# Optimization experiments

Measured on AMD Instinct MI355X. Metric: run time of the kernel, lower is better.

## Reference

```python
import jax, jax.numpy as jnp
import numpy as np

B, T = 64, 1024
S, O = 512, 32000


def setup_inputs() -> dict:
    key = jax.random.key(0)
    k1, k2, k3, k4 = jax.random.split(key, 4)
    return {
        "observations": jax.random.randint(k1, (B, T), 0, O),
        "state_transitions": jax.random.normal(k2, (S, S), dtype=jnp.float32),
        "observation_transitions": jax.random.normal(k3, (S, O), dtype=jnp.float32),
        "prior_states": jax.random.normal(k4, (S,), dtype=jnp.float32),
    }


def reference(observations, state_transitions, observation_transitions, prior_states):
    # Precompute log-softmaxed parameters once (torch code recomputed per step).
    log_trans = jax.nn.log_softmax(state_transitions, axis=-1)        # [S, S]
    log_obs = jax.nn.log_softmax(observation_transitions, axis=-1)    # [S, O]
    log_prior = jax.nn.log_softmax(prior_states)                      # [S]

    b = observations.shape[0]
    # torch code appends a terminal observation 0 at the end of each sequence
    obs_seq = jnp.concatenate(
        [observations, jnp.zeros((b, 1), dtype=observations.dtype)], axis=1
    )  # [B, T+1]

    # alpha_0[b, s] = log_obs[s, o_0(b)] + log_prior[s]
    alpha0 = log_obs[:, obs_seq[:, 0]].T + log_prior  # [B, S]

    def step(alpha, obs_t):
        # alpha[b, i] -> pred[b, j] = logsumexp_i(alpha[b, i] + log_trans[i, j])
        pred = jax.nn.logsumexp(alpha[:, :, None] + log_trans[None, :, :], axis=1)  # [B, S]
        new_alpha = log_obs[:, obs_t].T + pred  # [B, S]
        return new_alpha, None

    alpha, _ = jax.lax.scan(step, alpha0, obs_seq[:, 1:].T)  # scan over T steps
    return jax.nn.logsumexp(alpha, axis=1)  # [B]
```

## Files before the change

kernel.cpp:

```cpp
#include <hip/hip_runtime.h>
#include <hip/hip_bf16.h>
#include <cstdint>

#define SS 512
#define OBS_N 32000
#define TT 1024
#define BB 64

#define RPW 24
#define LDS_I2 64
#define LPW 8

typedef _Float16 h2 __attribute__((ext_vector_type(2)));

static __device__ __forceinline__ float wave_max(float v) {
#pragma unroll
  for (int m = 32; m >= 1; m >>= 1) v = fmaxf(v, __shfl_xor(v, m, 64));
  return v;
}
static __device__ __forceinline__ float wave_sum(float v) {
#pragma unroll
  for (int m = 32; m >= 1; m >>= 1) v += __shfl_xor(v, m, 64);
  return v;
}

__global__ __launch_bounds__(256) void prep_obs_lse(const float* __restrict__ ot,
                                                    float* __restrict__ lse) {
  const int s = blockIdx.x;
  const int tid = threadIdx.x;
  const float4* row = (const float4*)(ot + (size_t)s * OBS_N);
  __shared__ float redm[4];
  __shared__ float reds[4];

  float m = -INFINITY;
  for (int k = tid; k < OBS_N / 4; k += 256) {
    float4 v = row[k];
    m = fmaxf(m, fmaxf(fmaxf(v.x, v.y), fmaxf(v.z, v.w)));
  }
  m = wave_max(m);
  if ((tid & 63) == 0) redm[tid >> 6] = m;
  __syncthreads();
  m = fmaxf(fmaxf(redm[0], redm[1]), fmaxf(redm[2], redm[3]));

  float ssum = 0.f;
  for (int k = tid; k < OBS_N / 4; k += 256) {
    float4 v = row[k];
    ssum += __expf(v.x - m) + __expf(v.y - m) + __expf(v.z - m) + __expf(v.w - m);
  }
  ssum = wave_sum(ssum);
  if ((tid & 63) == 0) reds[tid >> 6] = ssum;
  __syncthreads();
  if (tid == 0) {
    float s4 = reds[0] + reds[1] + reds[2] + reds[3];
    lse[s] = m + __logf(s4);
  }
}

__global__ __launch_bounds__(512) void prep_trans(const float* __restrict__ st,
                                                  uint32_t* __restrict__ EP) {
  const int r = blockIdx.x;
  const int j = threadIdx.x;
  const int wv = j >> 6;
  float a0 = st[(size_t)(2 * r) * SS + j];
  float a1 = st[(size_t)(2 * r + 1) * SS + j];

  __shared__ float w0[8], w1[8], s0a[8], s1a[8];
  float m0 = wave_max(a0), m1 = wave_max(a1);
  if ((j & 63) == 0) { w0[wv] = m0; w1[wv] = m1; }
  __syncthreads();
  m0 = w0[0]; m1 = w1[0];
#pragma unroll
  for (int q = 1; q < 8; ++q) { m0 = fmaxf(m0, w0[q]); m1 = fmaxf(m1, w1[q]); }

  float e0 = __expf(a0 - m0), e1 = __expf(a1 - m1);
  float s0 = wave_sum(e0), s1 = wave_sum(e1);
  if ((j & 63) == 0) { s0a[wv] = s0; s1a[wv] = s1; }
  __syncthreads();
  s0 = 0.f; s1 = 0.f;
#pragma unroll
  for (int q = 0; q < 8; ++q) { s0 += s0a[q]; s1 += s1a[q]; }

  _Float16 h0 = (_Float16)(e0 / s0);
  _Float16 h1 = (_Float16)(e1 / s1);
  uint32_t u = ((uint32_t)__builtin_bit_cast(unsigned short, h1) << 16) |
               (uint32_t)__builtin_bit_cast(unsigned short, h0);
  EP[(size_t)r * SS + j] = u;
}

__global__ __launch_bounds__(512) void prep_prior(const float* __restrict__ pr,
                                                  float* __restrict__ lp) {
  const int j = threadIdx.x;
  const int wv = j >> 6;
  float a = pr[j];
  __shared__ float wm[8], ws[8];
  float m = wave_max(a);
  if ((j & 63) == 0) wm[wv] = m;
  __syncthreads();
  m = wm[0];
#pragma unroll
  for (int q = 1; q < 8; ++q) m = fmaxf(m, wm[q]);
  float e = __expf(a - m);
  float s = wave_sum(e);
  if ((j & 63) == 0) ws[wv] = s;
  __syncthreads();
  s = 0.f;
#pragma unroll
  for (int q = 0; q < 8; ++q) s += ws[q];
  lp[j] = a - m - __logf(s);
}

__global__ __launch_bounds__(512, 2) void hmm_main(
    const uint32_t* __restrict__ EP, const float* __restrict__ lse_obs,
    const float* __restrict__ lp, const int* __restrict__ obs,
    const float* __restrict__ ot, float* __restrict__ out) {
  __shared__ uint32_t eL[LDS_I2][64][8];
  __shared__ uint32_t ph32[SS / 2];
  __shared__ float pp[8][SS];
  __shared__ float wred[8];
  __shared__ float wsum[8];

  const int tid = threadIdx.x;
  const int w = tid >> 6;
  const int l = tid & 63;
  const int b = blockIdx.x;
  const int j = tid;

  uint32_t eR[RPW * 8];
#pragma unroll
  for (int p = 0; p < RPW; ++p)
#pragma unroll
    for (int k = 0; k < 8; ++k)
      eR[p * 8 + k] = EP[(size_t)(RPW * w + p) * SS + k * 64 + l];

  for (int q = 0; q < LDS_I2; ++q)
    eL[q][tid & 63][tid >> 6] = EP[(size_t)(192 + q) * SS + tid];

  const float lse_j = lse_obs[j];
  const float lpj = lp[j];
  const float* base_ot = ot + (size_t)j * OBS_N;
  const int* orow = obs + b * TT;

  const int o0 = orow[0];
  float alpha = base_ot[o0] - lse_j + lpj;

  int on = orow[1];
  float ot_next = base_ot[on];

  __syncthreads();

  for (int t = 1; t <= TT; ++t) {
    int o2 = (t <= TT - 2) ? orow[t + 1] : 0;
    float ot_pf = (t < TT) ? base_ot[o2] : 0.f;

    float m = wave_max(alpha);
    if (l == 0) wred[w] = m;
    __syncthreads();
    float M = wred[0];
#pragma unroll
    for (int q = 1; q < 8; ++q) M = fmaxf(M, wred[q]);

    float Pj = __expf(alpha - M);
    reinterpret_cast<unsigned short*>(ph32)[j] =
        __builtin_bit_cast(unsigned short, (_Float16)Pj);
    __syncthreads();

    h2 acc[8] = {};
#pragma unroll
    for (int p = 0; p < RPW; ++p) {
      h2 phv = __builtin_bit_cast(h2, ph32[RPW * w + p]);
#pragma unroll
      for (int k = 0; k < 8; ++k) {
        h2 ev = __builtin_bit_cast(h2, eR[p * 8 + k]);
        acc[k] += phv * ev;
      }
    }
#pragma unroll
    for (int q = 0; q < LPW; ++q) {
      h2 phv = __builtin_bit_cast(h2, ph32[192 + LPW * w + q]);
#pragma unroll
      for (int k = 0; k < 8; ++k) {
        h2 ev = __builtin_bit_cast(h2, eL[LPW * w + q][l][k]);
        acc[k] += phv * ev;
      }
    }
#pragma unroll
    for (int k = 0; k < 8; ++k)
      pp[w][k * 64 + l] = (float)acc[k].x + (float)acc[k].y;
    __syncthreads();

    float pred = 0.f;
#pragma unroll
    for (int q = 0; q < 8; ++q) pred += pp[q][j];
    alpha = M + __logf(pred) + (ot_next - lse_j);
    ot_next = ot_pf;
  }

  float m = wave_max(alpha);
  if (l == 0) wred[w] = m;
  __syncthreads();
  float M = wred[0];
#pragma unroll
  for (int q = 1; q < 8; ++q) M = fmaxf(M, wred[q]);
  float e = __expf(alpha - M);
  float s = wave_sum(e);
  if (l == 0) wsum[w] = s;
  __syncthreads();
  if (tid == 0) {
    float tot = 0.f;
#pragma unroll
    for (int q = 0; q < 8; ++q) tot += wsum[q];
    out[b] = M + __logf(tot);
  }
}

extern "C" void kernel_launch(void* const* d_in, const int* in_sizes, int n_in,
                              void* d_out, int out_size, void* d_ws, size_t ws_size,
                              hipStream_t stream) {
  const int* obs = (const int*)d_in[0];
  const float* st = (const float*)d_in[1];
  const float* ot = (const float*)d_in[2];
  const float* pr = (const float*)d_in[3];
  float* out = (float*)d_out;

  char* ws = (char*)d_ws;
  uint32_t* EP = (uint32_t*)ws;
  float* lse_obs = (float*)(ws + 524288);
  float* lprior = (float*)(ws + 524288 + 2048);

  prep_obs_lse<<<SS, 256, 0, stream>>>(ot, lse_obs);
  prep_trans<<<SS / 2, SS, 0, stream>>>(st, EP);
  prep_prior<<<1, SS, 0, stream>>>(pr, lprior);
  hmm_main<<<BB, SS, 0, stream>>>(EP, lse_obs, lprior, obs, ot, out);
}
```

Baseline: 2.032 ms.

## Use per-wave max normalization to cut barriers in HMM forward step

Each wave now normalizes its alpha slice by its own wave-local max, found with a DPP reduction, so the block-wide max barrier before the exp goes away. Each wave only reads its own probability slice, so a wave barrier is enough there. The cross-wave rescale is folded into the final reduction using the per-wave maxima, and wred/ppb are double-buffered so one block barrier per step suffices. The inner product moves to fdot2 with f32 accumulation and vectorized LDS reads, and partial sums are stored as fp16, which risks precision and overflow because the wave-local normalization is unbounded relative to the other waves.

```diff
diff --git a/kernel.cpp b/kernel.cpp
--- a/kernel.cpp
+++ b/kernel.cpp
@@ -8,8 +8,7 @@
 #define BB 64
 
 #define RPW 24
-#define LDS_I2 64
-#define LPW 8
+#define TPW 8
 
 typedef _Float16 h2 __attribute__((ext_vector_type(2)));
 
@@ -22,6 +21,39 @@
 #pragma unroll
   for (int m = 32; m >= 1; m >>= 1) v += __shfl_xor(v, m, 64);
   return v;
+}
+
+static __device__ __forceinline__ float wave_max_dpp(float x) {
+  int v = __builtin_bit_cast(int, x);
+#define DPP_STEP(ctrl)                                                        \
+  {                                                                           \
+    int t = __builtin_amdgcn_update_dpp(v, v, (ctrl), 0xf, 0xf, false);       \
+    v = __builtin_bit_cast(                                                   \
+        int, fmaxf(__builtin_bit_cast(float, v), __builtin_bit_cast(float, t)));\
+  }
+  DPP_STEP(0x111)
+  DPP_STEP(0x112)
+  DPP_STEP(0x114)
+  DPP_STEP(0x118)
+  DPP_STEP(0x142)
+  DPP_STEP(0x143)
+#undef DPP_STEP
+  return __builtin_bit_cast(float, __builtin_amdgcn_readlane(v, 63));
+}
+
+static __device__ __forceinline__ float dot2f(h2 a, h2 b, float c) {
+#if __has_builtin(__builtin_amdgcn_fdot2)
+  return __builtin_amdgcn_fdot2(a, b, c, false);
+#else
+  return c + (float)a.x * (float)b.x + (float)a.y * (float)b.y;
+#endif
+}
+
+static __device__ __forceinline__ h2 as_h2(uint32_t u) {
+  return __builtin_bit_cast(h2, u);
+}
+static __device__ __forceinline__ uint32_t sel4(const uint4& v, int s) {
+  return s == 0 ? v.x : s == 1 ? v.y : s == 2 ? v.z : v.w;
 }
 
 __global__ __launch_bounds__(256) void prep_obs_lse(const float* __restrict__ ot,
@@ -109,15 +141,15 @@
   lp[j] = a - m - __logf(s);
 }
 
-__global__ __launch_bounds__(512, 2) void hmm_main(
+__global__ __launch_bounds__(512, 1) void hmm_main(
     const uint32_t* __restrict__ EP, const float* __restrict__ lse_obs,
     const float* __restrict__ lp, const int* __restrict__ obs,
     const float* __restrict__ ot, float* __restrict__ out) {
-  __shared__ uint32_t eL[LDS_I2][64][8];
-  __shared__ uint32_t ph32[SS / 2];
-  __shared__ float pp[8][SS];
-  __shared__ float wred[8];
-  __shared__ float wsum[8];
+  __shared__ uint32_t eL[64][2][64][4];
+  __shared__ __align__(16) unsigned short ph16[SS];
+  __shared__ __align__(16) unsigned short ppb[2][8][SS];
+  __shared__ __align__(16) float wred[2][8];
+  __shared__ float fin_m[8], fin_s[8];
 
   const int tid = threadIdx.x;
   const int w = tid >> 6;
@@ -130,10 +162,19 @@
   for (int p = 0; p < RPW; ++p)
 #pragma unroll
     for (int k = 0; k < 8; ++k)
-      eR[p * 8 + k] = EP[(size_t)(RPW * w + p) * SS + k * 64 + l];
-
-  for (int q = 0; q < LDS_I2; ++q)
-    eL[q][tid & 63][tid >> 6] = EP[(size_t)(192 + q) * SS + tid];
+      eR[p * 8 + k] = EP[(size_t)(32 * w + p) * SS + k * 64 + l];
+
+  for (int idx = tid; idx < 64 * 2 * 64; idx += 512) {
+    int tq = idx >> 7;
+    int c = (idx >> 6) & 1;
+    int ll = idx & 63;
+    int pr = 32 * (tq >> 3) + RPW + (tq & 7);
+    const uint32_t* src = EP + (size_t)pr * SS + c * 256 + ll;
+    eL[tq][c][ll][0] = src[0];
+    eL[tq][c][ll][1] = src[64];
+    eL[tq][c][ll][2] = src[128];
+    eL[tq][c][ll][3] = src[192];
+  }
 
   const float lse_j = lse_obs[j];
   const float lpj = lp[j];
@@ -144,71 +185,98 @@
   float alpha = base_ot[o0] - lse_j + lpj;
 
   int on = orow[1];
-  float ot_next = base_ot[on];
+  float otv = base_ot[on];
 
   __syncthreads();
 
   for (int t = 1; t <= TT; ++t) {
+    const int par = t & 1;
+
     int o2 = (t <= TT - 2) ? orow[t + 1] : 0;
     float ot_pf = (t < TT) ? base_ot[o2] : 0.f;
 
-    float m = wave_max(alpha);
-    if (l == 0) wred[w] = m;
-    __syncthreads();
-    float M = wred[0];
-#pragma unroll
-    for (int q = 1; q < 8; ++q) M = fmaxf(M, wred[q]);
-
-    float Pj = __expf(alpha - M);
-    reinterpret_cast<unsigned short*>(ph32)[j] =
-        __builtin_bit_cast(unsigned short, (_Float16)Pj);
-    __syncthreads();
-
-    h2 acc[8] = {};
-#pragma unroll
-    for (int p = 0; p < RPW; ++p) {
-      h2 phv = __builtin_bit_cast(h2, ph32[RPW * w + p]);
-#pragma unroll
-      for (int k = 0; k < 8; ++k) {
-        h2 ev = __builtin_bit_cast(h2, eR[p * 8 + k]);
-        acc[k] += phv * ev;
+    float mw = wave_max_dpp(alpha);
+    if (l == 0) wred[par][w] = mw;
+
+    float Pj = __expf(alpha - mw);
+    ph16[j] = __builtin_bit_cast(unsigned short, (_Float16)Pj);
+    __builtin_amdgcn_wave_barrier();
+
+    float acc[8] = {0.f, 0.f, 0.f, 0.f, 0.f, 0.f, 0.f, 0.f};
+
+#pragma unroll
+    for (int qg = 0; qg < 2; ++qg) {
+      uint4 ph4 = *(const uint4*)&ph16[64 * w + 48 + 8 * qg];
+#pragma unroll
+      for (int s = 0; s < 4; ++s) {
+        const int q = 4 * qg + s;
+        h2 phv = as_h2(sel4(ph4, s));
+        const uint4 c0 = *(const uint4*)&eL[w * 8 + q][0][l][0];
+        const uint4 c1 = *(const uint4*)&eL[w * 8 + q][1][l][0];
+        acc[0] = dot2f(phv, as_h2(c0.x), acc[0]);
+        acc[1] = dot2f(phv, as_h2(c0.y), acc[1]);
+        acc[2] = dot2f(phv, as_h2(c0.z), acc[2]);
+        acc[3] = dot2f(phv, as_h2(c0.w), acc[3]);
+        acc[4] = dot2f(phv, as_h2(c1.x), acc[4]);
+        acc[5] = dot2f(phv, as_h2(c1.y), acc[5]);
+        acc[6] = dot2f(phv, as_h2(c1.z), acc[6]);
+        acc[7] = dot2f(phv, as_h2(c1.w), acc[7]);
       }
     }
-#pragma unroll
-    for (int q = 0; q < LPW; ++q) {
-      h2 phv = __builtin_bit_cast(h2, ph32[192 + LPW * w + q]);
-#pragma unroll
-      for (int k = 0; k < 8; ++k) {
-        h2 ev = __builtin_bit_cast(h2, eL[LPW * w + q][l][k]);
-        acc[k] += phv * ev;
+
+#pragma unroll
+    for (int g = 0; g < 6; ++g) {
+      uint4 ph4 = *(const uint4*)&ph16[64 * w + 8 * g];
+#pragma unroll
+      for (int s = 0; s < 4; ++s) {
+        const int p = 4 * g + s;
+        h2 phv = as_h2(sel4(ph4, s));
+#pragma unroll
+        for (int k = 0; k < 8; ++k)
+          acc[k] = dot2f(phv, as_h2(eR[p * 8 + k]), acc[k]);
       }
     }
+
 #pragma unroll
     for (int k = 0; k < 8; ++k)
-      pp[w][k * 64 + l] = (float)acc[k].x + (float)acc[k].y;
+      ppb[par][w][k * 64 + l] =
+          __builtin_bit_cast(unsigned short, (_Float16)acc[k]);
+
     __syncthreads();
 
+    const float4 wv0 = *(const float4*)&wred[par][0];
+    const float4 wv1 = *(const float4*)&wred[par][4];
+    float M = fmaxf(fmaxf(fmaxf(wv0.x, wv0.y), fmaxf(wv0.z, wv0.w)),
+                    fmaxf(fmaxf(wv1.x, wv1.y), fmaxf(wv1.z, wv1.w)));
+    float earg = wred[par][l & 7];
+    float ee = __expf(earg - M);
+
     float pred = 0.f;
 #pragma unroll
-    for (int q = 0; q < 8; ++q) pred += pp[q][j];
-    alpha = M + __logf(pred) + (ot_next - lse_j);
-    ot_next = ot_pf;
+    for (int q = 0; q < 8; ++q) {
+      float eq = __builtin_bit_cast(
+          float, __builtin_amdgcn_readlane(__builtin_bit_cast(int, ee), q));
+      float pq = (float)__builtin_bit_cast(_Float16, ppb[par][q][j]);
+      pred = fmaf(eq, pq, pred);
+    }
+    alpha = M + __logf(pred) + (otv - lse_j);
+    otv = ot_pf;
   }
 
   float m = wave_max(alpha);
-  if (l == 0) wred[w] = m;
-  __syncthreads();
-  float M = wred[0];
-#pragma unroll
-  for (int q = 1; q < 8; ++q) M = fmaxf(M, wred[q]);
+  if (l == 0) fin_m[w] = m;
+  __syncthreads();
+  float M = fin_m[0];
+#pragma unroll
+  for (int q = 1; q < 8; ++q) M = fmaxf(M, fin_m[q]);
   float e = __expf(alpha - M);
   float s = wave_sum(e);
-  if (l == 0) wsum[w] = s;
+  if (l == 0) fin_s[w] = s;
   __syncthreads();
   if (tid == 0) {
     float tot = 0.f;
 #pragma unroll
-    for (int q = 0; q < 8; ++q) tot += wsum[q];
+    for (int q = 0; q < 8; ++q) tot += fin_s[q];
     out[b] = M + __logf(tot);
   }
 }
```

After: 1.864 ms. -8.3%, faster.
